# Performance work log

Hardware: AMD Instinct MI355X
Metric: run time of the kernel (lower is better)

## Reference

```python
import jax, jax.numpy as jnp
import numpy as np

IN_F, OUT_F, BLOCK, NBLK = 1024, 4096, 256, 16
TOPK = NBLK // 4  # 4, as in forward: n_blocks // 4


def setup_inputs() -> dict:
    key = jax.random.key(0)
    ks = jax.random.split(key, 7)
    s = 1.0 / np.sqrt(IN_F)
    s2 = 1.0 / np.sqrt(OUT_F)
    return {
        "x": jax.random.normal(ks[0], (4, 4096, IN_F), jnp.float32),
        "router_w": jax.random.uniform(ks[1], (NBLK, IN_F), jnp.float32, -s, s),
        "router_b": jax.random.uniform(ks[2], (NBLK,), jnp.float32, -s, s),
        "w1": jax.random.uniform(ks[3], (OUT_F, IN_F), jnp.float32, -s, s),
        "b1": jax.random.uniform(ks[4], (OUT_F,), jnp.float32, -s, s),
        "w2": jax.random.uniform(ks[5], (IN_F, OUT_F), jnp.float32, -s2, s2),
        "b2": jax.random.uniform(ks[6], (IN_F,), jnp.float32, -s2, s2),
    }


def reference(x, router_w, router_b, w1, b1, w2, b2):
    x_shape = x.shape
    xf = x.reshape(-1, IN_F)  # [N, d]
    n = xf.shape[0]
    # router: Linear + softmax, then top-k block selection per token
    prob = jax.nn.softmax(xf @ router_w.T + router_b, axis=-1)  # [N, n_blocks]
    _, idx = jax.lax.top_k(prob, TOPK)  # [N, k]
    mask = jnp.zeros((n, NBLK), bool).at[jnp.arange(n)[:, None], idx].set(True)
    # RoutedLinearRow: per-block fc1, zeros at unselected blocks
    w1b = w1.reshape(NBLK, BLOCK, IN_F)
    b1b = b1.reshape(NBLK, BLOCK)
    h = jnp.einsum('nd,ibd->nib', xf, w1b) + b1b  # [N, n_blocks, block]
    h = jnp.where(mask[:, :, None], h, jnp.zeros((), h.dtype))
    h = jax.nn.relu(h)
    # RoutedLinearCol: only selected blocks contribute
    w2b = w2.reshape(IN_F, NBLK, BLOCK)
    y = jnp.einsum('nib,dib->nd', jnp.where(mask[:, :, None], h, 0.0), w2b) + b2
    return y.reshape(x_shape)
```

## Files before the change

kernel.cpp:

```cpp
#include <hip/hip_runtime.h>
#include <hip/hip_bf16.h>

#define NTOK   16384
#define INF    1024
#define OUTF   4096
#define NBLK   16
#define BLKSZ  256
#define KTOP   4

typedef short bf16x8 __attribute__((ext_vector_type(8)));
typedef float f32x4 __attribute__((ext_vector_type(4)));
typedef unsigned short u16x8 __attribute__((ext_vector_type(8)));

__device__ __forceinline__ unsigned short f2bf(float f) {
  unsigned u = __float_as_uint(f);
  u += 0x7FFFu + ((u >> 16) & 1u);
  return (unsigned short)(u >> 16);
}

__device__ __forceinline__ void load_lds16(const void* g, void* l) {
  __builtin_amdgcn_global_load_lds(
      (const __attribute__((address_space(1))) unsigned int*)g,
      (__attribute__((address_space(3))) unsigned int*)l, 16, 0, 0);
}

__device__ __forceinline__ double shfl_xor_d(double v, int m) {
  long long l = __double_as_longlong(v);
  int lo = (int)(l & 0xFFFFFFFFll), hi = (int)(l >> 32);
  lo = __shfl_xor(lo, m);
  hi = __shfl_xor(hi, m);
  return __longlong_as_double(((long long)hi << 32) | (unsigned long long)(unsigned)lo);
}

__device__ __forceinline__ int pi_perm(int j) {
  return (j & 128) | ((j & 7) << 4) | ((j >> 3) & 15);
}

__global__ __launch_bounds__(256) void k_cvt_router(
    const float* __restrict__ x, const float* __restrict__ rw,
    const float* __restrict__ rb, const float* __restrict__ w1,
    const float* __restrict__ w2, const float* __restrict__ b1,
    unsigned* __restrict__ tok_blocks, unsigned* __restrict__ counts,
    unsigned short* __restrict__ xb, unsigned short* __restrict__ w1b,
    unsigned short* __restrict__ w2p, float* __restrict__ b1p) {
  __shared__ float4 rwl[4096];
  const int tid = threadIdx.x;
  const float4* rw4 = (const float4*)rw;
  for (int i = tid; i < 4096; i += 256) rwl[i] = rw4[i];
  __syncthreads();

  const int n = blockIdx.x * 32 + (tid >> 3);
  const int q = tid & 7;
  double p[16];
#pragma unroll
  for (int j = 0; j < 16; ++j) p[j] = 0.0;
  const float4* xr = (const float4*)(x + (size_t)n * INF);
  ushort4* xbr = (ushort4*)(xb + (size_t)n * INF);
#pragma unroll 4
  for (int i = 0; i < 32; ++i) {
    const int d4 = q + i * 8;
    const float4 xv = xr[d4];
    ushort4 o;
    o.x = f2bf(xv.x); o.y = f2bf(xv.y); o.z = f2bf(xv.z); o.w = f2bf(xv.w);
    xbr[d4] = o;
#pragma unroll
    for (int j = 0; j < 16; ++j) {
      const float4 wv = rwl[j * 256 + d4];
      p[j] = fma((double)xv.x, (double)wv.x, p[j]);
      p[j] = fma((double)xv.y, (double)wv.y, p[j]);
      p[j] = fma((double)xv.z, (double)wv.z, p[j]);
      p[j] = fma((double)xv.w, (double)wv.w, p[j]);
    }
  }
#pragma unroll
  for (int j = 0; j < 16; ++j) {
    double v = p[j];
    v += shfl_xor_d(v, 1);
    v += shfl_xor_d(v, 2);
    v += shfl_xor_d(v, 4);
    p[j] = v + (double)rb[j];
  }

  __syncthreads();
  unsigned* hist = (unsigned*)rwl;
  if (tid < 16) hist[tid] = 0;
  __syncthreads();

  if (q == 0) {
    unsigned packed = 0;
#pragma unroll
    for (int j = 0; j < 16; ++j) {
      int r = 0;
#pragma unroll
      for (int j2 = 0; j2 < 16; ++j2)
        r += (int)((p[j2] > p[j]) | ((p[j2] == p[j]) & (j2 < j)));
      if (r < KTOP) packed |= (unsigned)j << (8 * r);
    }
    tok_blocks[n] = packed;
    atomicAdd(&hist[packed & 15u], 1u);
    atomicAdd(&hist[(packed >> 8) & 15u], 1u);
    atomicAdd(&hist[(packed >> 16) & 15u], 1u);
    atomicAdd(&hist[(packed >> 24) & 15u], 1u);
  }
  __syncthreads();
  if (tid < 16 && hist[tid]) atomicAdd(&counts[tid], hist[tid]);

  const size_t stride = (size_t)gridDim.x * 256;
  for (size_t i = (size_t)blockIdx.x * 256 + tid; i < 1573376; i += stride) {
    if (i < 1048576) {
      float4 v = ((const float4*)w1)[i];
      ushort4 o;
      o.x = f2bf(v.x); o.y = f2bf(v.y); o.z = f2bf(v.z); o.w = f2bf(v.w);
      ((ushort4*)w1b)[i] = o;
    } else if (i < 1572864) {
      const size_t g = i - 1048576;
      const int d = (int)(g >> 9);
      const int rest = (int)(g & 511);
      const int jg = rest * 8;
      const int blk = jg >> 8;
      const int j0 = jg & 255;
      const float* src = w2 + (size_t)d * 4096 + blk * 256;
      u16x8 o;
#pragma unroll
      for (int ni = 0; ni < 8; ++ni) o[ni] = f2bf(src[pi_perm(j0 + ni)]);
      *(u16x8*)(w2p + (size_t)d * 4096 + jg) = o;
    } else {
      const int idx = (int)(i - 1572864);
      const int jg = idx * 8;
      const int blk = jg >> 8;
      const int j0 = jg & 255;
      const float* src = b1 + blk * 256;
      float o[8];
#pragma unroll
      for (int ni = 0; ni < 8; ++ni) o[ni] = src[pi_perm(j0 + ni)];
      float4* dst = (float4*)(b1p + jg);
      dst[0] = make_float4(o[0], o[1], o[2], o[3]);
      dst[1] = make_float4(o[4], o[5], o[6], o[7]);
    }
  }
}

__global__ __launch_bounds__(256) void k_build(
    const unsigned* __restrict__ tok_blocks, const unsigned* __restrict__ counts,
    unsigned* __restrict__ alloc, unsigned short* __restrict__ list) {
  unsigned offl[16];
  {
    unsigned o = 0;
#pragma unroll
    for (int i = 0; i < 16; ++i) { offl[i] = o; o += (counts[i] + 127u) & ~127u; }
  }
  const int n = blockIdx.x * 256 + threadIdx.x;
  const unsigned packed = tok_blocks[n];
  const int lane = threadIdx.x & 63;
#pragma unroll
  for (int b = 0; b < 16; ++b) {
    int r = -1;
#pragma unroll
    for (int q = 0; q < 4; ++q)
      if (((packed >> (8 * q)) & 15u) == (unsigned)b) r = q;
    unsigned long long m = __ballot(r >= 0);
    if (m) {
      int leader = __ffsll((unsigned long long)m) - 1;
      unsigned base = 0;
      if (lane == leader) base = offl[b] + atomicAdd(&alloc[b], (unsigned)__popcll(m));
      base = (unsigned)__shfl((int)base, leader);
      if (r >= 0) {
        unsigned pos = base + (unsigned)__popcll(m & ((1ull << lane) - 1ull));
        list[pos] = (unsigned short)(n | (r << 14));
      }
    }
  }
}

__global__ __launch_bounds__(512, 1) void k_ffn(
    const unsigned short* __restrict__ xb, const unsigned short* __restrict__ w1b,
    const unsigned short* __restrict__ w2p, const float* __restrict__ b1p,
    const unsigned short* __restrict__ list, const unsigned* __restrict__ counts,
    unsigned short* __restrict__ part) {
  __shared__ __align__(16) char lds[163840];
  char* const As0 = lds + 65536;
  char* const As1 = lds + 81920;
  char* const Bs0 = lds + 98304;
  char* const Bs1 = lds + 131072;

  const int bid0 = blockIdx.x;
  const int bid = (bid0 & 7) * 256 + (bid0 >> 3);
  const int blk = bid >> 7;
  const int tile = bid & 127;
  unsigned cnt = 0, goffBase = 0;
  {
    unsigned o = 0;
#pragma unroll
    for (int i = 0; i < 16; ++i) {
      const unsigned c = counts[i];
      if (i == blk) { cnt = c; goffBase = o; }
      o += (c + 127u) & ~127u;
    }
  }
  if ((unsigned)(tile * 128) >= cnt) return;
  const unsigned goff = goffBase + tile * 128;
  const int rem = (int)cnt - tile * 128;

  const int tid = threadIdx.x;
  const int lane = tid & 63;
  const int wid = tid >> 6;
  const int wr = wid >> 1;
  const int wc = wid & 1;
  const int asl = tid & 7;
  const int c16 = lane & 15;

  const unsigned tok0 = list[goff + (tid >> 3)] & 0x3FFFu;
  const unsigned tok1 = list[goff + 64 + (tid >> 3)] & 0x3FFFu;
  const int arow0 = tid >> 3;
  const int arow1 = 64 + arow0;

  unsigned ep[2][4];
#pragma unroll
  for (int mi = 0; mi < 2; ++mi)
#pragma unroll
    for (int i = 0; i < 4; ++i)
      ep[mi][i] = list[goff + wr * 32 + mi * 16 + (lane >> 4) * 4 + i];

#define STAGE_A(buf, k0)                                                        \
  {                                                                             \
    load_lds16(xb + (size_t)tok0 * INF + (k0) + (asl ^ (arow0 & 7)) * 8,        \
               (buf) + (wid * 64) * 16);                                        \
    load_lds16(xb + (size_t)tok1 * INF + (k0) + (asl ^ (arow1 & 7)) * 8,        \
               (buf) + (512 + wid * 64) * 16);                                  \
  }

#define STAGE_B1(buf, k0)                                                       \
  _Pragma("unroll")                                                             \
  for (int r = 0; r < 4; ++r) {                                                 \
    const int row = (r * 512 + tid) >> 3;                                       \
    load_lds16(w1b + ((size_t)(blk * 256 + row)) * INF + (k0) +                 \
                   (asl ^ (row & 7)) * 8,                                       \
               (buf) + (r * 512 + wid * 64) * 16);                              \
  }

#define COMPUTE_A(abuf, bbuf)                                                   \
  _Pragma("unroll")                                                             \
  for (int ks = 0; ks < 2; ++ks) {                                              \
    const int kc = ks * 4 + (lane >> 4);                                        \
    bf16x8 a[2], b[8];                                                          \
    _Pragma("unroll")                                                           \
    for (int mi = 0; mi < 2; ++mi) {                                            \
      const int row = wr * 32 + mi * 16 + c16;                                  \
      a[mi] = *(const bf16x8*)((abuf) + row * 128 + ((kc ^ (row & 7)) << 4));   \
    }                                                                           \
    _Pragma("unroll")                                                           \
    for (int ni = 0; ni < 8; ++ni) {                                            \
      const int row = wc * 128 + ni * 16 + c16;                                 \
      b[ni] = *(const bf16x8*)((bbuf) + row * 128 + ((kc ^ (row & 7)) << 4));   \
    }                                                                           \
    _Pragma("unroll")                                                           \
    for (int mi = 0; mi < 2; ++mi)                                              \
      _Pragma("unroll")                                                         \
      for (int ni = 0; ni < 8; ++ni)                                            \
        acc[mi][ni] =                                                           \
            __builtin_amdgcn_mfma_f32_16x16x32_bf16(a[mi], b[ni], acc[mi][ni], 0, 0, 0); \
  }

  f32x4 acc[2][8] = {};
  STAGE_A(As0, 0);
  STAGE_B1(Bs0, 0);
  __syncthreads();
#pragma unroll 1
  for (int kk = 0; kk < 8; ++kk) {
    const int k0 = kk * 128;
    STAGE_A(As1, k0 + 64);
    STAGE_B1(Bs1, k0 + 64);
    COMPUTE_A(As0, Bs0);
    __syncthreads();
    if (kk < 7) {
      STAGE_A(As0, k0 + 128);
      STAGE_B1(Bs0, k0 + 128);
    }
    COMPUTE_A(As1, Bs1);
    __syncthreads();
  }

#define STAGE_B2(buf, it)                                                       \
  {                                                                             \
    const int ns2 = (it) >> 2, k02 = ((it) & 3) * 64;                           \
    _Pragma("unroll")                                                           \
    for (int r = 0; r < 4; ++r) {                                               \
      const int row = (r * 512 + tid) >> 3;                                     \
      load_lds16(w2p + (size_t)(ns2 * 256 + row) * OUTF + blk * 256 + k02 +     \
                     (asl ^ (row & 7)) * 8,                                     \
                 (buf) + (r * 512 + wid * 64) * 16);                            \
    }                                                                           \
  }

#define COMPUTE_B(bbuf, kg)                                                     \
  _Pragma("unroll")                                                             \
  for (int ks = 0; ks < 2; ++ks) {                                              \
    const int kc = ks * 4 + (lane >> 4);                                        \
    bf16x8 b[8];                                                                \
    _Pragma("unroll")                                                           \
    for (int ni = 0; ni < 8; ++ni) {                                            \
      const int row = wc * 128 + ni * 16 + c16;                                 \
      b[ni] = *(const bf16x8*)((bbuf) + row * 128 + ((kc ^ (row & 7)) << 4));   \
    }                                                                           \
    _Pragma("unroll")                                                           \
    for (int mi = 0; mi < 2; ++mi)                                              \
      _Pragma("unroll")                                                         \
      for (int ni = 0; ni < 8; ++ni)                                            \
        acc2[mi][ni] = __builtin_amdgcn_mfma_f32_16x16x32_bf16(                 \
            pa[mi][ks][kg], b[ni], acc2[mi][ni], 0, 0, 0);                      \
  }

  STAGE_B2(Bs0, 0);

  {
    const float4* bp = (const float4*)(b1p + blk * 256 + wc * 128 + c16 * 8);
    const float4 bv0 = bp[0], bv1 = bp[1];
    const float bvv[8] = {bv0.x, bv0.y, bv0.z, bv0.w, bv1.x, bv1.y, bv1.z, bv1.w};
    const int chunk = wc * 16 + c16;
    const int cslot = (chunk & ~7);
    const int clow  = (chunk & 7);
#pragma unroll
    for (int mi = 0; mi < 2; ++mi) {
#pragma unroll
      for (int i = 0; i < 4; ++i) {
        const int row = wr * 32 + mi * 16 + (lane >> 4) * 4 + i;
        u16x8 wv;
#pragma unroll
        for (int ni = 0; ni < 8; ++ni) {
          float v = acc[mi][ni][i] + bvv[ni];
          v = v > 0.f ? v : 0.f;
          wv[ni] = f2bf(v);
        }
        *(u16x8*)(lds + row * 512 + ((cslot | (clow ^ (row & 7))) << 4)) = wv;
      }
    }
  }
  __syncthreads();

  bf16x8 pa[2][2][4];
#pragma unroll
  for (int mi = 0; mi < 2; ++mi) {
    const int row = wr * 32 + mi * 16 + c16;
#pragma unroll
    for (int ks = 0; ks < 2; ++ks) {
      const int kc = ks * 4 + (lane >> 4);
#pragma unroll
      for (int kg = 0; kg < 4; ++kg)
        pa[mi][ks][kg] = *(const bf16x8*)(lds + row * 512 + kg * 128 +
                                          ((kc ^ (row & 7)) << 4));
    }
  }

#pragma unroll 1
  for (int ns = 0; ns < 4; ++ns) {
    f32x4 acc2[2][8] = {};
    const int it0 = ns * 4;
    STAGE_B2(Bs1, it0 + 1);
    COMPUTE_B(Bs0, 0);
    __syncthreads();
    STAGE_B2(Bs0, it0 + 2);
    COMPUTE_B(Bs1, 1);
    __syncthreads();
    STAGE_B2(Bs1, it0 + 3);
    COMPUTE_B(Bs0, 2);
    __syncthreads();
    if (ns < 3) STAGE_B2(Bs0, it0 + 4);
    COMPUTE_B(Bs1, 3);
    __syncthreads();
#pragma unroll
    for (int mi = 0; mi < 2; ++mi) {
#pragma unroll
      for (int i = 0; i < 4; ++i) {
        const int row = wr * 32 + mi * 16 + (lane >> 4) * 4 + i;
        if (row < rem) {
          const unsigned e = ep[mi][i];
          u16x8 wv;
#pragma unroll
          for (int ni = 0; ni < 8; ++ni) wv[ni] = f2bf(acc2[mi][ni][i]);
          *(u16x8*)(part + ((size_t)(e & 0x3FFFu) * 4 + (e >> 14)) * 1024 +
                    ns * 256 + wc * 128 + c16 * 8) = wv;
        }
      }
    }
  }
#undef STAGE_A
#undef STAGE_B1
#undef STAGE_B2
#undef COMPUTE_A
#undef COMPUTE_B
}

__global__ __launch_bounds__(256) void k_reduce(const unsigned short* __restrict__ part,
                                                const float* __restrict__ b2,
                                                float* __restrict__ out) {
  __shared__ float lds[8 * 1028];
  const int tid = threadIdx.x;
  const int tok0 = blockIdx.x * 8;
  const int tok_l = tid >> 5;
  const int l32 = tid & 31;
  const unsigned short* pbase = part + (size_t)(tok0 + tok_l) * 4096;

#pragma unroll
  for (int g = 0; g < 4; ++g) {
    const int idx = g * 32 + l32;
    const int p0 = idx * 8;
    float s[8] = {0.f, 0.f, 0.f, 0.f, 0.f, 0.f, 0.f, 0.f};
#pragma unroll
    for (int sl = 0; sl < 4; ++sl) {
      u16x8 v = *(const u16x8*)(pbase + sl * 1024 + p0);
#pragma unroll
      for (int j = 0; j < 8; ++j)
        s[j] += __uint_as_float((unsigned)(unsigned short)v[j] << 16);
    }
    const int ns = idx >> 5, wcb = (idx >> 4) & 1, cc = idx & 15;
#pragma unroll
    for (int ni = 0; ni < 8; ++ni)
      lds[tok_l * 1028 + ns * 256 + wcb * 128 + ni * 16 + cc] = s[ni];
  }
  __syncthreads();
  const float4 b2v = ((const float4*)b2)[tid];
#pragma unroll
  for (int r = 0; r < 8; ++r) {
    f32x4 lv = *(f32x4*)&lds[r * 1028 + tid * 4];
    float4 o = make_float4(lv[0] + b2v.x, lv[1] + b2v.y, lv[2] + b2v.z, lv[3] + b2v.w);
    *(float4*)(out + (size_t)(tok0 + r) * 1024 + tid * 4) = o;
  }
}

extern "C" void kernel_launch(void* const* d_in, const int* in_sizes, int n_in,
                              void* d_out, int out_size, void* d_ws, size_t ws_size,
                              hipStream_t stream) {
  const float* x  = (const float*)d_in[0];
  const float* rw = (const float*)d_in[1];
  const float* rb = (const float*)d_in[2];
  const float* w1 = (const float*)d_in[3];
  const float* b1 = (const float*)d_in[4];
  const float* w2 = (const float*)d_in[5];
  const float* b2 = (const float*)d_in[6];
  float* out = (float*)d_out;

  char* ws = (char*)d_ws;
  unsigned short* part = (unsigned short*)(ws);
  unsigned short* xb   = (unsigned short*)(ws + 134217728);
  unsigned short* w1b  = (unsigned short*)(ws + 167772160);
  unsigned short* w2p  = (unsigned short*)(ws + 176160768);
  unsigned* tokb       = (unsigned*)(ws + 184549376);
  unsigned short* list = (unsigned short*)(ws + 184614912);
  float* b1p           = (float*)(ws + 184750080);
  unsigned* counts     = (unsigned*)(ws + 184766464);
  unsigned* alloc      = (unsigned*)(ws + 184766528);

  hipMemsetAsync(ws + 184766464, 0, 128, stream);
  k_cvt_router<<<dim3(512), dim3(256), 0, stream>>>(x, rw, rb, w1, w2, b1, tokb,
                                                    counts, xb, w1b, w2p, b1p);
  k_build<<<dim3(64), dim3(256), 0, stream>>>(tokb, counts, alloc, list);
  k_ffn<<<dim3(2048), dim3(512), 0, stream>>>(xb, w1b, w2p, b1p, list, counts, part);
  k_reduce<<<dim3(2048), dim3(256), 0, stream>>>(part, b2, out);
}
```

Measured before the change: 259.5 us.

## Remap routed FFN tiles to cap work at 512 blocks plus tail passes

Computes a global compact tile index across experts so only the first 512 real tiles are processed by their natural blocks, and any overflow tiles are assigned as a second pass to low-numbered blocks. The kernel body is wrapped in a loop over up to two work items per block. This aims to avoid a sparse extra wave of blocks for tiles beyond one full round on the CUs, at the cost of extra prefix computation and serialized passes in some blocks.

```diff
diff --git a/kernel.cpp b/kernel.cpp
--- a/kernel.cpp
+++ b/kernel.cpp
@@ -185,21 +185,23 @@
 
   const int bid0 = blockIdx.x;
   const int bid = (bid0 & 7) * 256 + (bid0 >> 3);
-  const int blk = bid >> 7;
-  const int tile = bid & 127;
-  unsigned cnt = 0, goffBase = 0;
-  {
-    unsigned o = 0;
-#pragma unroll
-    for (int i = 0; i < 16; ++i) {
-      const unsigned c = counts[i];
-      if (i == blk) { cnt = c; goffBase = o; }
-      o += (c + 127u) & ~127u;
-    }
-  }
-  if ((unsigned)(tile * 128) >= cnt) return;
-  const unsigned goff = goffBase + tile * 128;
-  const int rem = (int)cnt - tile * 128;
+  const int blk0 = bid >> 7;
+  const int tile0 = bid & 127;
+
+  unsigned r0 = 0xFFFFFFFFu, T_tot = 0;
+#pragma unroll
+  for (int e = 0; e < 16; ++e) {
+    const unsigned tc = (counts[e] + 127u) >> 7;
+    if (e == blk0 && (unsigned)tile0 < tc) r0 = T_tot + (unsigned)tile0;
+    T_tot += tc;
+  }
+  const unsigned tail = T_tot > 512u ? T_tot - 512u : 0u;
+  const unsigned w0 = (r0 != 0xFFFFFFFFu && r0 < 512u) ? r0 : 0xFFFFFFFFu;
+  const unsigned w1 = ((unsigned)bid0 < tail) ? 512u + (unsigned)bid0 : 0xFFFFFFFFu;
+  int nw = 0;
+  if (w0 != 0xFFFFFFFFu) nw = 1;
+  if (w1 != 0xFFFFFFFFu) nw = (nw == 1) ? 2 : -2;
+  if (nw == 0) return;
 
   const int tid = threadIdx.x;
   const int lane = tid & 63;
@@ -209,17 +211,37 @@
   const int asl = tid & 7;
   const int c16 = lane & 15;
 
-  const unsigned tok0 = list[goff + (tid >> 3)] & 0x3FFFu;
-  const unsigned tok1 = list[goff + 64 + (tid >> 3)] & 0x3FFFu;
-  const int arow0 = tid >> 3;
-  const int arow1 = 64 + arow0;
-
-  unsigned ep[2][4];
-#pragma unroll
-  for (int mi = 0; mi < 2; ++mi)
-#pragma unroll
-    for (int i = 0; i < 4; ++i)
-      ep[mi][i] = list[goff + wr * 32 + mi * 16 + (lane >> 4) * 4 + i];
+  const int npass = (nw == 2) ? 2 : 1;
+
+#pragma unroll 1
+  for (int pw = 0; pw < npass; ++pw) {
+    const unsigned w = (nw == -2) ? w1 : (pw == 0 ? w0 : w1);
+    int blk = 0; unsigned tileIn = 0, goffB = 0, cblk = 0;
+    {
+      unsigned T = 0, o = 0;
+#pragma unroll
+      for (int e = 0; e < 16; ++e) {
+        const unsigned c = counts[e];
+        const unsigned tc = (c + 127u) >> 7;
+        if (w >= T && w < T + tc) { blk = e; tileIn = w - T; goffB = o; cblk = c; }
+        T += tc;
+        o += (c + 127u) & ~127u;
+      }
+    }
+    const unsigned goff = goffB + tileIn * 128u;
+    const int rem = (int)cblk - (int)(tileIn * 128u);
+
+    const unsigned tok0 = list[goff + (tid >> 3)] & 0x3FFFu;
+    const unsigned tok1 = list[goff + 64 + (tid >> 3)] & 0x3FFFu;
+    const int arow0 = tid >> 3;
+    const int arow1 = 64 + arow0;
+
+    unsigned ep[2][4];
+#pragma unroll
+    for (int mi = 0; mi < 2; ++mi)
+#pragma unroll
+      for (int i = 0; i < 4; ++i)
+        ep[mi][i] = list[goff + wr * 32 + mi * 16 + (lane >> 4) * 4 + i];
 
 #define STAGE_A(buf, k0)                                                        \
   {                                                                             \
@@ -261,24 +283,24 @@
             __builtin_amdgcn_mfma_f32_16x16x32_bf16(a[mi], b[ni], acc[mi][ni], 0, 0, 0); \
   }
 
-  f32x4 acc[2][8] = {};
-  STAGE_A(As0, 0);
-  STAGE_B1(Bs0, 0);
-  __syncthreads();
+    f32x4 acc[2][8] = {};
+    STAGE_A(As0, 0);
+    STAGE_B1(Bs0, 0);
+    __syncthreads();
 #pragma unroll 1
-  for (int kk = 0; kk < 8; ++kk) {
-    const int k0 = kk * 128;
-    STAGE_A(As1, k0 + 64);
-    STAGE_B1(Bs1, k0 + 64);
-    COMPUTE_A(As0, Bs0);
-    __syncthreads();
-    if (kk < 7) {
-      STAGE_A(As0, k0 + 128);
-      STAGE_B1(Bs0, k0 + 128);
-    }
-    COMPUTE_A(As1, Bs1);
-    __syncthreads();
-  }
+    for (int kk = 0; kk < 8; ++kk) {
+      const int k0 = kk * 128;
+      STAGE_A(As1, k0 + 64);
+      STAGE_B1(Bs1, k0 + 64);
+      COMPUTE_A(As0, Bs0);
+      __syncthreads();
+      if (kk < 7) {
+        STAGE_A(As0, k0 + 128);
+        STAGE_B1(Bs0, k0 + 128);
+      }
+      COMPUTE_A(As1, Bs1);
+      __syncthreads();
+    }
 
 #define STAGE_B2(buf, it)                                                       \
   {                                                                             \
@@ -310,84 +332,85 @@
             pa[mi][ks][kg], b[ni], acc2[mi][ni], 0, 0, 0);                      \
   }
 
-  STAGE_B2(Bs0, 0);
-
-  {
-    const float4* bp = (const float4*)(b1p + blk * 256 + wc * 128 + c16 * 8);
-    const float4 bv0 = bp[0], bv1 = bp[1];
-    const float bvv[8] = {bv0.x, bv0.y, bv0.z, bv0.w, bv1.x, bv1.y, bv1.z, bv1.w};
-    const int chunk = wc * 16 + c16;
-    const int cslot = (chunk & ~7);
-    const int clow  = (chunk & 7);
+    STAGE_B2(Bs0, 0);
+
+    {
+      const float4* bp = (const float4*)(b1p + blk * 256 + wc * 128 + c16 * 8);
+      const float4 bv0 = bp[0], bv1 = bp[1];
+      const float bvv[8] = {bv0.x, bv0.y, bv0.z, bv0.w, bv1.x, bv1.y, bv1.z, bv1.w};
+      const int chunk = wc * 16 + c16;
+      const int cslot = (chunk & ~7);
+      const int clow  = (chunk & 7);
+#pragma unroll
+      for (int mi = 0; mi < 2; ++mi) {
+#pragma unroll
+        for (int i = 0; i < 4; ++i) {
+          const int row = wr * 32 + mi * 16 + (lane >> 4) * 4 + i;
+          u16x8 wv;
+#pragma unroll
+          for (int ni = 0; ni < 8; ++ni) {
+            float v = acc[mi][ni][i] + bvv[ni];
+            v = v > 0.f ? v : 0.f;
+            wv[ni] = f2bf(v);
+          }
+          *(u16x8*)(lds + row * 512 + ((cslot | (clow ^ (row & 7))) << 4)) = wv;
+        }
+      }
+    }
+    __syncthreads();
+
+    bf16x8 pa[2][2][4];
 #pragma unroll
     for (int mi = 0; mi < 2; ++mi) {
-#pragma unroll
-      for (int i = 0; i < 4; ++i) {
-        const int row = wr * 32 + mi * 16 + (lane >> 4) * 4 + i;
-        u16x8 wv;
-#pragma unroll
-        for (int ni = 0; ni < 8; ++ni) {
-          float v = acc[mi][ni][i] + bvv[ni];
-          v = v > 0.f ? v : 0.f;
-          wv[ni] = f2bf(v);
+      const int row = wr * 32 + mi * 16 + c16;
+#pragma unroll
+      for (int ks = 0; ks < 2; ++ks) {
+        const int kc = ks * 4 + (lane >> 4);
+#pragma unroll
+        for (int kg = 0; kg < 4; ++kg)
+          pa[mi][ks][kg] = *(const bf16x8*)(lds + row * 512 + kg * 128 +
+                                            ((kc ^ (row & 7)) << 4));
+      }
+    }
+
+#pragma unroll 1
+    for (int ns = 0; ns < 4; ++ns) {
+      f32x4 acc2[2][8] = {};
+      const int it0 = ns * 4;
+      STAGE_B2(Bs1, it0 + 1);
+      COMPUTE_B(Bs0, 0);
+      __syncthreads();
+      STAGE_B2(Bs0, it0 + 2);
+      COMPUTE_B(Bs1, 1);
+      __syncthreads();
+      STAGE_B2(Bs1, it0 + 3);
+      COMPUTE_B(Bs0, 2);
+      __syncthreads();
+      if (ns < 3) STAGE_B2(Bs0, it0 + 4);
+      COMPUTE_B(Bs1, 3);
+      __syncthreads();
+#pragma unroll
+      for (int mi = 0; mi < 2; ++mi) {
+#pragma unroll
+        for (int i = 0; i < 4; ++i) {
+          const int row = wr * 32 + mi * 16 + (lane >> 4) * 4 + i;
+          if (row < rem) {
+            const unsigned e = ep[mi][i];
+            u16x8 wv;
+#pragma unroll
+            for (int ni = 0; ni < 8; ++ni) wv[ni] = f2bf(acc2[mi][ni][i]);
+            *(u16x8*)(part + ((size_t)(e & 0x3FFFu) * 4 + (e >> 14)) * 1024 +
+                      ns * 256 + wc * 128 + c16 * 8) = wv;
+          }
         }
-        *(u16x8*)(lds + row * 512 + ((cslot | (clow ^ (row & 7))) << 4)) = wv;
-      }
-    }
-  }
-  __syncthreads();
-
-  bf16x8 pa[2][2][4];
-#pragma unroll
-  for (int mi = 0; mi < 2; ++mi) {
-    const int row = wr * 32 + mi * 16 + c16;
-#pragma unroll
-    for (int ks = 0; ks < 2; ++ks) {
-      const int kc = ks * 4 + (lane >> 4);
-#pragma unroll
-      for (int kg = 0; kg < 4; ++kg)
-        pa[mi][ks][kg] = *(const bf16x8*)(lds + row * 512 + kg * 128 +
-                                          ((kc ^ (row & 7)) << 4));
-    }
-  }
-
-#pragma unroll 1
-  for (int ns = 0; ns < 4; ++ns) {
-    f32x4 acc2[2][8] = {};
-    const int it0 = ns * 4;
-    STAGE_B2(Bs1, it0 + 1);
-    COMPUTE_B(Bs0, 0);
-    __syncthreads();
-    STAGE_B2(Bs0, it0 + 2);
-    COMPUTE_B(Bs1, 1);
-    __syncthreads();
-    STAGE_B2(Bs1, it0 + 3);
-    COMPUTE_B(Bs0, 2);
-    __syncthreads();
-    if (ns < 3) STAGE_B2(Bs0, it0 + 4);
-    COMPUTE_B(Bs1, 3);
-    __syncthreads();
-#pragma unroll
-    for (int mi = 0; mi < 2; ++mi) {
-#pragma unroll
-      for (int i = 0; i < 4; ++i) {
-        const int row = wr * 32 + mi * 16 + (lane >> 4) * 4 + i;
-        if (row < rem) {
-          const unsigned e = ep[mi][i];
-          u16x8 wv;
-#pragma unroll
-          for (int ni = 0; ni < 8; ++ni) wv[ni] = f2bf(acc2[mi][ni][i]);
-          *(u16x8*)(part + ((size_t)(e & 0x3FFFu) * 4 + (e >> 14)) * 1024 +
-                    ns * 256 + wc * 128 + c16 * 8) = wv;
-        }
-      }
-    }
-  }
+      }
+    }
 #undef STAGE_A
 #undef STAGE_B1
 #undef STAGE_B2
 #undef COMPUTE_A
 #undef COMPUTE_B
+  }
 }
 
 __global__ __launch_bounds__(256) void k_reduce(const unsigned short* __restrict__ part,
```

After: 280.1 us. 7.9% more time.
